# Kernel optimization log

Hardware: AMD Instinct MI355X
Metric: run time of the kernel (lower is better)

The kernel has to match this reference:

```python
import jax, jax.numpy as jnp
import numpy as np

B, D, K, H, E, Z = 64, 25000, 16, 128, 256, 32


def setup_inputs() -> dict:
    key = jax.random.key(0)
    ks = jax.random.split(key, 10)
    s = 0.02
    return {
        "x": jax.random.normal(ks[0], (B, D), jnp.float32),
        "mask": jax.random.randint(ks[1], (B, D), 0, 2, jnp.int32),
        "feat_emb": jax.random.normal(ks[2], (D, K), jnp.float32),          # feature_embedding [D,K]
        "feat_bias": jnp.zeros((D, 1), jnp.float32),                        # feature_bias [D,1]
        "W1": jax.random.normal(ks[3], (1 + K + 1, H), jnp.float32) * s,    # h_layer linear 1 (in,out)
        "b1": jnp.zeros((H,), jnp.float32),
        "W2": jax.random.normal(ks[4], (H, K), jnp.float32) * s,            # h_layer linear 2
        "b2": jnp.zeros((K,), jnp.float32),
        "We1": jax.random.normal(ks[5], (K, E), jnp.float32) * s,           # encoder_mlp linear 1
        "be1": jnp.zeros((E,), jnp.float32),
        "We2": jax.random.normal(ks[6], (E, 2 * Z), jnp.float32) * s,       # encoder_mlp linear 2
        "be2": jnp.zeros((2 * Z,), jnp.float32),
    }


def reference(x, mask, feat_emb, feat_bias, W1, b1, W2, b2, We1, be1, We2, be2):
    b, d = x.shape
    k = feat_emb.shape[1]
    # Build per-(sample, feature) input rows: [x_bd, F_d(K), bias_d] -> [B, D, 1+K+1]
    h_in = jnp.concatenate(
        [
            x[:, :, None],
            jnp.broadcast_to(feat_emb[None, :, :], (b, d, k)),
            jnp.broadcast_to(feat_bias[None, :, :], (b, d, 1)),
        ],
        axis=-1,
    )
    # Shared small MLP (h_layer), dropout is identity at rate 0.0
    h = jax.nn.relu(h_in @ W1 + b1)          # [B, D, H]
    h = jax.nn.relu(h @ W2 + b2)             # [B, D, K]
    # Masked sum pooling over features
    c = jnp.sum(h * mask.astype(h.dtype)[:, :, None], axis=1)  # [B, K]
    # encoder_mlp
    enc = jax.nn.relu(c @ We1 + be1) @ We2 + be2                # [B, 2Z]
    mu, logvar = jnp.split(enc, 2, axis=-1)
    return mu, logvar
```

## Files before the change

### kernel.cpp

```cpp
#include <hip/hip_runtime.h>
#include <hip/hip_bf16.h>

#define B 64
#define D 25000
#define K 16
#define H 128
#define E 256
#define Z 32
#define DTILE 10
#define NBLK (D / DTILE)
#define NREP 8
#define NTILE ((D + 63) / 64)

#define REP_BYTES (NREP * B * K * 4)
#define HI_OFF    REP_BYTES
#define W1F_OFF   (HI_OFF + H * K * 2)
#define XT_OFF    (W1F_OFF + 8 * 64 * 8 * 2)
#define MT_OFF    (XT_OFF + D * B * 2)

typedef __attribute__((ext_vector_type(8))) _Float16 half8;
typedef __attribute__((ext_vector_type(4))) _Float16 hv4;
typedef __attribute__((ext_vector_type(2))) _Float16 hv2;
typedef __attribute__((ext_vector_type(4))) float f32x4;

__global__ __launch_bounds__(256) void prep_kernel(
    const float* __restrict__ x, const int* __restrict__ mask,
    const float* __restrict__ W1, const float* __restrict__ b1,
    const float* __restrict__ W2, float* __restrict__ rep,
    _Float16* __restrict__ hiW2, _Float16* __restrict__ w1f,
    _Float16* __restrict__ xTh, _Float16* __restrict__ mTh)
{
    const int t = threadIdx.x;
    const int bid = blockIdx.x;
    if (bid < NREP) {
        for (int i = t; i < B * K; i += 256) rep[bid * B * K + i] = 0.f;
    } else if (bid == NREP) {
        for (int i = t; i < H * K; i += 256) {
            int j = i & 7, n = (i >> 3) & 15, g = (i >> 7) & 3, s = i >> 9;
            int k = s * 32 + g * 8 + j;
            hiW2[i] = (_Float16)W2[k * K + n];
        }
    } else if (bid == NREP + 1) {
        for (int i = t; i < 8 * 64 * 8; i += 256) {
            int j = i & 7, lane = (i >> 3) & 63, c = i >> 9;
            int g = lane >> 4, n = lane & 15;
            int k = g * 8 + j, h = c * 16 + n;
            float v;
            if (k < 16)       v = W1[(1 + k) * H + h];
            else if (k == 16) v = W1[17 * H + h];
            else if (k == 17) v = b1[h];
            else              v = 0.f;
            w1f[i] = (_Float16)v;
        }
    } else {
        __shared__ float tx[64 * 65];
        __shared__ float tm[64 * 65];
        const int dt0 = (bid - NREP - 2) * 64;
        const int dn  = min(64, D - dt0);
        for (int i = t; i < 64 * 64; i += 256) {
            int bb = i >> 6, dd = i & 63;
            if (dd < dn) {
                tx[dd * 65 + bb] = x[(size_t)bb * D + dt0 + dd];
                tm[dd * 65 + bb] = (float)mask[(size_t)bb * D + dt0 + dd];
            }
        }
        __syncthreads();
        for (int i = t; i < dn * 64; i += 256) {
            int dd = i >> 6, bb = i & 63;
            xTh[(size_t)(dt0 + dd) * 64 + bb] = (_Float16)tx[dd * 65 + bb];
            mTh[(size_t)(dt0 + dd) * 64 + bb] = (_Float16)tm[dd * 65 + bb];
        }
    }
}

__global__ __launch_bounds__(256) void partial_main_kernel(
    const float* __restrict__ feat_emb, const float* __restrict__ feat_bias,
    const float* __restrict__ W1, const float* __restrict__ b2,
    const _Float16* __restrict__ hiW2, const _Float16* __restrict__ w1f,
    const _Float16* __restrict__ xTh, const _Float16* __restrict__ mTh,
    float* __restrict__ rep)
{
    __shared__ __align__(16) _Float16 sGh[DTILE * H];
    __shared__ __align__(16) _Float16 sXh[DTILE * B];
    __shared__ __align__(16) _Float16 sMh[DTILE * B];

    const int t    = threadIdx.x;
    const int d0   = blockIdx.x * DTILE;
    const int lane = t & 63;
    const int wv   = t >> 6;
    const int g    = lane >> 4;
    const int n    = lane & 15;

    {
        const unsigned* xs = (const unsigned*)(xTh + (size_t)d0 * B);
        const unsigned* ms = (const unsigned*)(mTh + (size_t)d0 * B);
        unsigned* xd = (unsigned*)sXh;
        unsigned* md = (unsigned*)sMh;
        for (int i = t; i < DTILE * B / 2; i += 256) { xd[i] = xs[i]; md[i] = ms[i]; }
    }

    {
        const int m  = n;
        const int dA = min(d0 + m, D - 1);
        union AF { half8 v; _Float16 e[8]; } af;
        if (g < 2) {
            const float4* fe = (const float4*)&feat_emb[(size_t)dA * K + g * 8];
            float4 u0 = fe[0], u1 = fe[1];
            af.e[0] = (_Float16)u0.x; af.e[1] = (_Float16)u0.y;
            af.e[2] = (_Float16)u0.z; af.e[3] = (_Float16)u0.w;
            af.e[4] = (_Float16)u1.x; af.e[5] = (_Float16)u1.y;
            af.e[6] = (_Float16)u1.z; af.e[7] = (_Float16)u1.w;
        } else if (g == 2) {
            af.e[0] = (_Float16)feat_bias[dA];
            af.e[1] = (_Float16)1.f;
            #pragma unroll
            for (int j = 2; j < 8; ++j) af.e[j] = (_Float16)0.f;
        } else {
            #pragma unroll
            for (int j = 0; j < 8; ++j) af.e[j] = (_Float16)0.f;
        }
        #pragma unroll
        for (int cc = 0; cc < 2; ++cc) {
            const int c = wv * 2 + cc;
            half8 bf = *(const half8*)(w1f + (((c << 6) + lane) << 3));
            f32x4 C = {0.f, 0.f, 0.f, 0.f};
            C = __builtin_amdgcn_mfma_f32_16x16x32_f16(af.v, bf, C, 0, 0, 0);
            #pragma unroll
            for (int r = 0; r < 4; ++r) {
                const int m2 = g * 4 + r;
                if (m2 < DTILE) sGh[m2 * H + c * 16 + n] = (_Float16)C[r];
            }
        }
    }

    half8 Bf[4];
    #pragma unroll
    for (int s = 0; s < 4; ++s)
        Bf[s] = *(const half8*)(hiW2 + (((s * 4 + g) * 16 + n) << 3));
    hv2 w0h[4][4];
    #pragma unroll
    for (int s = 0; s < 4; ++s) {
        const float4* wp = (const float4*)&W1[s * 32 + g * 8];
        float4 a0 = wp[0], a1 = wp[1];
        w0h[s][0] = (hv2){(_Float16)a0.x, (_Float16)a0.y};
        w0h[s][1] = (hv2){(_Float16)a0.z, (_Float16)a0.w};
        w0h[s][2] = (hv2){(_Float16)a1.x, (_Float16)a1.y};
        w0h[s][3] = (hv2){(_Float16)a1.z, (_Float16)a1.w};
    }
    const float b2n = b2[n];
    const hv2 zeroh = {(_Float16)0.f, (_Float16)0.f};
    __syncthreads();

    const int sample = wv * 16 + n;
    hv2 xh[DTILE / 2];
    #pragma unroll
    for (int i = 0; i < DTILE / 2; ++i)
        xh[i] = (hv2){sXh[(2 * i) * B + sample], sXh[(2 * i + 1) * B + sample]};

    f32x4 cacc = {0.f, 0.f, 0.f, 0.f};
    const int moff = wv * 16 + g * 4;
    const _Float16* gb0 = sGh + g * 8;

    #pragma unroll
    for (int i = 0; i < DTILE / 2; ++i) {
        const int dd0 = 2 * i, dd1 = 2 * i + 1;
        const hv2 xa = {xh[i].x, xh[i].x};
        const hv2 xb = {xh[i].y, xh[i].y};
        f32x4 c1a = {b2n, b2n, b2n, b2n};
        f32x4 c1b = {b2n, b2n, b2n, b2n};
        #pragma unroll
        for (int s = 0; s < 4; ++s) {
            union GA { half8 v; hv2 p[4]; };
            GA ga, gb, A0, A1;
            ga.v = *(const half8*)(gb0 + dd0 * H + s * 32);
            gb.v = *(const half8*)(gb0 + dd1 * H + s * 32);
            #pragma unroll
            for (int p = 0; p < 4; ++p) {
                hv2 h0 = __builtin_elementwise_fma(xa, w0h[s][p], ga.p[p]);
                hv2 h1 = __builtin_elementwise_fma(xb, w0h[s][p], gb.p[p]);
                A0.p[p] = __builtin_elementwise_max(h0, zeroh);
                A1.p[p] = __builtin_elementwise_max(h1, zeroh);
            }
            c1a = __builtin_amdgcn_mfma_f32_16x16x32_f16(A0.v, Bf[s], c1a, 0, 0, 0);
            c1b = __builtin_amdgcn_mfma_f32_16x16x32_f16(A1.v, Bf[s], c1b, 0, 0, 0);
        }
        hv4 m0 = *(const hv4*)&sMh[dd0 * B + moff];
        hv4 m1 = *(const hv4*)&sMh[dd1 * B + moff];
        cacc[0] = fmaf((float)m0.x, fmaxf(c1a[0], 0.f), fmaf((float)m1.x, fmaxf(c1b[0], 0.f), cacc[0]));
        cacc[1] = fmaf((float)m0.y, fmaxf(c1a[1], 0.f), fmaf((float)m1.y, fmaxf(c1b[1], 0.f), cacc[1]));
        cacc[2] = fmaf((float)m0.z, fmaxf(c1a[2], 0.f), fmaf((float)m1.z, fmaxf(c1b[2], 0.f), cacc[2]));
        cacc[3] = fmaf((float)m0.w, fmaxf(c1a[3], 0.f), fmaf((float)m1.w, fmaxf(c1b[3], 0.f), cacc[3]));
    }

    float* crep = rep + (size_t)(blockIdx.x & (NREP - 1)) * (B * K);
    #pragma unroll
    for (int r = 0; r < 4; ++r)
        atomicAdd(&crep[(moff + r) * K + n], cacc[r]);
}

__global__ __launch_bounds__(256) void partial_enc_kernel(
    const float* __restrict__ rep, const float* __restrict__ We1,
    const float* __restrict__ be1, const float* __restrict__ We2,
    const float* __restrict__ be2, float* __restrict__ out)
{
    const int b = blockIdx.x;
    const int t = threadIdx.x;
    __shared__ float sc[K];
    __shared__ float st1[E];
    __shared__ float red[256];

    {
        const int k = t & 15, grp = t >> 4;
        red[t] = (grp < NREP) ? rep[grp * (B * K) + b * K + k] : 0.f;
    }
    __syncthreads();
    if (t < K) {
        float s2 = 0.f;
        #pragma unroll
        for (int q = 0; q < 16; ++q) s2 += red[q * 16 + t];
        sc[t] = s2;
    }
    __syncthreads();

    {
        float acc = be1[t];
        #pragma unroll
        for (int k = 0; k < K; ++k)
            acc = fmaf(sc[k], We1[k * E + t], acc);
        st1[t] = fmaxf(acc, 0.f);
    }
    __syncthreads();

    const int j = t & 63, seg = t >> 6;
    float acc = 0.f;
    #pragma unroll 4
    for (int e = seg * 64; e < seg * 64 + 64; ++e)
        acc = fmaf(st1[e], We2[e * 64 + j], acc);
    red[t] = acc;
    __syncthreads();

    if (t < 64) {
        float v = red[j] + red[64 + j] + red[128 + j] + red[192 + j] + be2[j];
        if (j < Z) out[b * Z + j] = v;
        else       out[B * Z + b * Z + (j - Z)] = v;
    }
}

extern "C" void kernel_launch(void* const* d_in, const int* in_sizes, int n_in,
                              void* d_out, int out_size, void* d_ws, size_t ws_size,
                              hipStream_t stream) {
    const float* x         = (const float*)d_in[0];
    const int*   mask      = (const int*)  d_in[1];
    const float* feat_emb  = (const float*)d_in[2];
    const float* feat_bias = (const float*)d_in[3];
    const float* W1        = (const float*)d_in[4];
    const float* b1        = (const float*)d_in[5];
    const float* W2        = (const float*)d_in[6];
    const float* b2        = (const float*)d_in[7];
    const float* We1       = (const float*)d_in[8];
    const float* be1       = (const float*)d_in[9];
    const float* We2       = (const float*)d_in[10];
    const float* be2       = (const float*)d_in[11];

    float*     rep  = (float*)d_ws;
    _Float16*  hiW2 = (_Float16*)((char*)d_ws + HI_OFF);
    _Float16*  w1f  = (_Float16*)((char*)d_ws + W1F_OFF);
    _Float16*  xTh  = (_Float16*)((char*)d_ws + XT_OFF);
    _Float16*  mTh  = (_Float16*)((char*)d_ws + MT_OFF);

    prep_kernel<<<NREP + 2 + NTILE, 256, 0, stream>>>(
        x, mask, W1, b1, W2, rep, hiW2, w1f, xTh, mTh);
    partial_main_kernel<<<NBLK, 256, 0, stream>>>(
        feat_emb, feat_bias, W1, b2, hiW2, w1f, xTh, mTh, rep);
    partial_enc_kernel<<<B, 256, 0, stream>>>(
        rep, We1, be1, We2, be2, (float*)d_out);
}
```

Measured before the change: 112.9 us.

## Fuse transpose prep into main kernel with double-buffered 16-feature tiles

Removes the separate prep kernel that transposed x/mask to fp16 workspace and pre-swizzled the weights. Each block now loads x and mask directly with vectorized global reads, builds the weight fragments in registers, and processes two 16-feature tiles with double-buffered shared memory so the next tile is staged while the current one is computed. The rep buffer is zeroed with hipMemsetAsync instead. This cuts a full write-and-read pass over the transposed inputs and one launch, but adds per-block weight setup and strided global reads of x/mask.

```diff
diff --git a/kernel.cpp b/kernel.cpp
--- a/kernel.cpp
+++ b/kernel.cpp
@@ -1,5 +1,4 @@
 #include <hip/hip_runtime.h>
-#include <hip/hip_bf16.h>
 
 #define B 64
 #define D 25000
@@ -7,102 +6,109 @@
 #define H 128
 #define E 256
 #define Z 32
-#define DTILE 10
-#define NBLK (D / DTILE)
+#define DTILE 16
+#define NT_TILES 1563
+#define TILES_PER_BLK 2
+#define NPB 782
 #define NREP 8
-#define NTILE ((D + 63) / 64)
+#define XSTR 68
 
 #define REP_BYTES (NREP * B * K * 4)
-#define HI_OFF    REP_BYTES
-#define W1F_OFF   (HI_OFF + H * K * 2)
-#define XT_OFF    (W1F_OFF + 8 * 64 * 8 * 2)
-#define MT_OFF    (XT_OFF + D * B * 2)
 
 typedef __attribute__((ext_vector_type(8))) _Float16 half8;
 typedef __attribute__((ext_vector_type(4))) _Float16 hv4;
 typedef __attribute__((ext_vector_type(2))) _Float16 hv2;
 typedef __attribute__((ext_vector_type(4))) float f32x4;
 
-__global__ __launch_bounds__(256) void prep_kernel(
+__global__ __launch_bounds__(256) void main_kernel(
     const float* __restrict__ x, const int* __restrict__ mask,
+    const float* __restrict__ feat_emb, const float* __restrict__ feat_bias,
     const float* __restrict__ W1, const float* __restrict__ b1,
-    const float* __restrict__ W2, float* __restrict__ rep,
-    _Float16* __restrict__ hiW2, _Float16* __restrict__ w1f,
-    _Float16* __restrict__ xTh, _Float16* __restrict__ mTh)
+    const float* __restrict__ W2, const float* __restrict__ b2,
+    float* __restrict__ rep)
 {
-    const int t = threadIdx.x;
-    const int bid = blockIdx.x;
-    if (bid < NREP) {
-        for (int i = t; i < B * K; i += 256) rep[bid * B * K + i] = 0.f;
-    } else if (bid == NREP) {
-        for (int i = t; i < H * K; i += 256) {
-            int j = i & 7, n = (i >> 3) & 15, g = (i >> 7) & 3, s = i >> 9;
-            int k = s * 32 + g * 8 + j;
-            hiW2[i] = (_Float16)W2[k * K + n];
-        }
-    } else if (bid == NREP + 1) {
-        for (int i = t; i < 8 * 64 * 8; i += 256) {
-            int j = i & 7, lane = (i >> 3) & 63, c = i >> 9;
-            int g = lane >> 4, n = lane & 15;
-            int k = g * 8 + j, h = c * 16 + n;
+    __shared__ __align__(16) _Float16 sGh[2][DTILE * H];
+    __shared__ __align__(16) _Float16 sXh[2][DTILE * XSTR];
+    __shared__ __align__(16) _Float16 sMh[2][DTILE * XSTR];
+
+    const int t    = threadIdx.x;
+    const int lane = t & 63;
+    const int wv   = t >> 6;
+    const int g    = lane >> 4;
+    const int n    = lane & 15;
+
+    half8 Bf[4];
+    #pragma unroll
+    for (int s = 0; s < 4; ++s) {
+        union { half8 v; _Float16 e[8]; } u;
+        #pragma unroll
+        for (int j = 0; j < 8; ++j)
+            u.e[j] = (_Float16)W2[(s * 32 + g * 8 + j) * K + n];
+        Bf[s] = u.v;
+    }
+    hv2 w0h[4][4];
+    #pragma unroll
+    for (int s = 0; s < 4; ++s) {
+        const float4* wp = (const float4*)&W1[s * 32 + g * 8];
+        float4 a0 = wp[0], a1 = wp[1];
+        w0h[s][0] = (hv2){(_Float16)a0.x, (_Float16)a0.y};
+        w0h[s][1] = (hv2){(_Float16)a0.z, (_Float16)a0.w};
+        w0h[s][2] = (hv2){(_Float16)a1.x, (_Float16)a1.y};
+        w0h[s][3] = (hv2){(_Float16)a1.z, (_Float16)a1.w};
+    }
+    half8 bfG[2];
+    #pragma unroll
+    for (int cc = 0; cc < 2; ++cc) {
+        const int h = (wv * 2 + cc) * 16 + n;
+        union { half8 v; _Float16 e[8]; } u;
+        #pragma unroll
+        for (int j = 0; j < 8; ++j) {
+            const int k = g * 8 + j;
             float v;
             if (k < 16)       v = W1[(1 + k) * H + h];
             else if (k == 16) v = W1[17 * H + h];
             else if (k == 17) v = b1[h];
             else              v = 0.f;
-            w1f[i] = (_Float16)v;
-        }
-    } else {
-        __shared__ float tx[64 * 65];
-        __shared__ float tm[64 * 65];
-        const int dt0 = (bid - NREP - 2) * 64;
-        const int dn  = min(64, D - dt0);
-        for (int i = t; i < 64 * 64; i += 256) {
-            int bb = i >> 6, dd = i & 63;
-            if (dd < dn) {
-                tx[dd * 65 + bb] = x[(size_t)bb * D + dt0 + dd];
-                tm[dd * 65 + bb] = (float)mask[(size_t)bb * D + dt0 + dd];
+            u.e[j] = (_Float16)v;
+        }
+        bfG[cc] = u.v;
+    }
+    const float b2n = b2[n];
+    const hv2 zeroh = {(_Float16)0.f, (_Float16)0.f};
+    const int moff = wv * 16 + g * 4;
+    const int sample = wv * 16 + n;
+
+    const int t0 = blockIdx.x * TILES_PER_BLK;
+    const int t1 = min(t0 + TILES_PER_BLK, NT_TILES);
+
+    auto STAGE = [&](int buf, int tile) {
+        const int bb = t >> 2;
+        const int dd = (t & 3) * 4;
+        const int dg = tile * DTILE + dd;
+        float xv[4], mv[4];
+        if (dg + 4 <= D) {
+            float4 xx = *(const float4*)&x[(size_t)bb * D + dg];
+            int4   mm = *(const int4*)&mask[(size_t)bb * D + dg];
+            xv[0] = xx.x; xv[1] = xx.y; xv[2] = xx.z; xv[3] = xx.w;
+            mv[0] = (float)mm.x; mv[1] = (float)mm.y; mv[2] = (float)mm.z; mv[3] = (float)mm.w;
+        } else {
+            #pragma unroll
+            for (int i = 0; i < 4; ++i) {
+                const int dgi = dg + i;
+                xv[i] = (dgi < D) ? x[(size_t)bb * D + dgi] : 0.f;
+                mv[i] = (dgi < D) ? (float)mask[(size_t)bb * D + dgi] : 0.f;
             }
         }
-        __syncthreads();
-        for (int i = t; i < dn * 64; i += 256) {
-            int dd = i >> 6, bb = i & 63;
-            xTh[(size_t)(dt0 + dd) * 64 + bb] = (_Float16)tx[dd * 65 + bb];
-            mTh[(size_t)(dt0 + dd) * 64 + bb] = (_Float16)tm[dd * 65 + bb];
-        }
-    }
-}
-
-__global__ __launch_bounds__(256) void partial_main_kernel(
-    const float* __restrict__ feat_emb, const float* __restrict__ feat_bias,
-    const float* __restrict__ W1, const float* __restrict__ b2,
-    const _Float16* __restrict__ hiW2, const _Float16* __restrict__ w1f,
-    const _Float16* __restrict__ xTh, const _Float16* __restrict__ mTh,
-    float* __restrict__ rep)
-{
-    __shared__ __align__(16) _Float16 sGh[DTILE * H];
-    __shared__ __align__(16) _Float16 sXh[DTILE * B];
-    __shared__ __align__(16) _Float16 sMh[DTILE * B];
-
-    const int t    = threadIdx.x;
-    const int d0   = blockIdx.x * DTILE;
-    const int lane = t & 63;
-    const int wv   = t >> 6;
-    const int g    = lane >> 4;
-    const int n    = lane & 15;
-
-    {
-        const unsigned* xs = (const unsigned*)(xTh + (size_t)d0 * B);
-        const unsigned* ms = (const unsigned*)(mTh + (size_t)d0 * B);
-        unsigned* xd = (unsigned*)sXh;
-        unsigned* md = (unsigned*)sMh;
-        for (int i = t; i < DTILE * B / 2; i += 256) { xd[i] = xs[i]; md[i] = ms[i]; }
-    }
-
-    {
-        const int m  = n;
-        const int dA = min(d0 + m, D - 1);
-        union AF { half8 v; _Float16 e[8]; } af;
+        #pragma unroll
+        for (int i = 0; i < 4; ++i) {
+            sXh[buf][(dd + i) * XSTR + bb] = (_Float16)xv[i];
+            sMh[buf][(dd + i) * XSTR + bb] = (_Float16)mv[i];
+        }
+    };
+
+    auto GCOMP = [&](int buf, int tile) {
+        const int dA = min(tile * DTILE + n, D - 1);
+        union { half8 v; _Float16 e[8]; } af;
         if (g < 2) {
             const float4* fe = (const float4*)&feat_emb[(size_t)dA * K + g * 8];
             float4 u0 = fe[0], u1 = fe[1];
@@ -121,75 +127,63 @@
         }
         #pragma unroll
         for (int cc = 0; cc < 2; ++cc) {
-            const int c = wv * 2 + cc;
-            half8 bf = *(const half8*)(w1f + (((c << 6) + lane) << 3));
             f32x4 C = {0.f, 0.f, 0.f, 0.f};
-            C = __builtin_amdgcn_mfma_f32_16x16x32_f16(af.v, bf, C, 0, 0, 0);
-            #pragma unroll
-            for (int r = 0; r < 4; ++r) {
-                const int m2 = g * 4 + r;
-                if (m2 < DTILE) sGh[m2 * H + c * 16 + n] = (_Float16)C[r];
+            C = __builtin_amdgcn_mfma_f32_16x16x32_f16(af.v, bfG[cc], C, 0, 0, 0);
+            #pragma unroll
+            for (int r = 0; r < 4; ++r)
+                sGh[buf][(g * 4 + r) * H + (wv * 2 + cc) * 16 + n] = (_Float16)C[r];
+        }
+    };
+
+    f32x4 cacc = {0.f, 0.f, 0.f, 0.f};
+
+    STAGE(0, t0);
+    GCOMP(0, t0);
+    __syncthreads();
+
+    int cur = 0;
+    for (int tt = t0; tt < t1; ++tt) {
+        if (tt + 1 < t1) { STAGE(cur ^ 1, tt + 1); GCOMP(cur ^ 1, tt + 1); }
+
+        hv2 xh[DTILE / 2];
+        #pragma unroll
+        for (int i = 0; i < DTILE / 2; ++i)
+            xh[i] = (hv2){sXh[cur][(2 * i) * XSTR + sample],
+                          sXh[cur][(2 * i + 1) * XSTR + sample]};
+        const _Float16* gb0 = sGh[cur] + g * 8;
+
+        #pragma unroll
+        for (int i = 0; i < DTILE / 2; ++i) {
+            const int dd0 = 2 * i, dd1 = 2 * i + 1;
+            const hv2 xa = {xh[i].x, xh[i].x};
+            const hv2 xb = {xh[i].y, xh[i].y};
+            f32x4 c1a = {b2n, b2n, b2n, b2n};
+            f32x4 c1b = {b2n, b2n, b2n, b2n};
+            #pragma unroll
+            for (int s = 0; s < 4; ++s) {
+                union GA { half8 v; hv2 p[4]; };
+                GA ga, gb, A0, A1;
+                ga.v = *(const half8*)(gb0 + dd0 * H + s * 32);
+                gb.v = *(const half8*)(gb0 + dd1 * H + s * 32);
+                #pragma unroll
+                for (int p = 0; p < 4; ++p) {
+                    hv2 h0 = __builtin_elementwise_fma(xa, w0h[s][p], ga.p[p]);
+                    hv2 h1 = __builtin_elementwise_fma(xb, w0h[s][p], gb.p[p]);
+                    A0.p[p] = __builtin_elementwise_max(h0, zeroh);
+                    A1.p[p] = __builtin_elementwise_max(h1, zeroh);
+                }
+                c1a = __builtin_amdgcn_mfma_f32_16x16x32_f16(A0.v, Bf[s], c1a, 0, 0, 0);
+                c1b = __builtin_amdgcn_mfma_f32_16x16x32_f16(A1.v, Bf[s], c1b, 0, 0, 0);
             }
-        }
-    }
-
-    half8 Bf[4];
-    #pragma unroll
-    for (int s = 0; s < 4; ++s)
-        Bf[s] = *(const half8*)(hiW2 + (((s * 4 + g) * 16 + n) << 3));
-    hv2 w0h[4][4];
-    #pragma unroll
-    for (int s = 0; s < 4; ++s) {
-        const float4* wp = (const float4*)&W1[s * 32 + g * 8];
-        float4 a0 = wp[0], a1 = wp[1];
-        w0h[s][0] = (hv2){(_Float16)a0.x, (_Float16)a0.y};
-        w0h[s][1] = (hv2){(_Float16)a0.z, (_Float16)a0.w};
-        w0h[s][2] = (hv2){(_Float16)a1.x, (_Float16)a1.y};
-        w0h[s][3] = (hv2){(_Float16)a1.z, (_Float16)a1.w};
-    }
-    const float b2n = b2[n];
-    const hv2 zeroh = {(_Float16)0.f, (_Float16)0.f};
-    __syncthreads();
-
-    const int sample = wv * 16 + n;
-    hv2 xh[DTILE / 2];
-    #pragma unroll
-    for (int i = 0; i < DTILE / 2; ++i)
-        xh[i] = (hv2){sXh[(2 * i) * B + sample], sXh[(2 * i + 1) * B + sample]};
-
-    f32x4 cacc = {0.f, 0.f, 0.f, 0.f};
-    const int moff = wv * 16 + g * 4;
-    const _Float16* gb0 = sGh + g * 8;
-
-    #pragma unroll
-    for (int i = 0; i < DTILE / 2; ++i) {
-        const int dd0 = 2 * i, dd1 = 2 * i + 1;
-        const hv2 xa = {xh[i].x, xh[i].x};
-        const hv2 xb = {xh[i].y, xh[i].y};
-        f32x4 c1a = {b2n, b2n, b2n, b2n};
-        f32x4 c1b = {b2n, b2n, b2n, b2n};
-        #pragma unroll
-        for (int s = 0; s < 4; ++s) {
-            union GA { half8 v; hv2 p[4]; };
-            GA ga, gb, A0, A1;
-            ga.v = *(const half8*)(gb0 + dd0 * H + s * 32);
-            gb.v = *(const half8*)(gb0 + dd1 * H + s * 32);
-            #pragma unroll
-            for (int p = 0; p < 4; ++p) {
-                hv2 h0 = __builtin_elementwise_fma(xa, w0h[s][p], ga.p[p]);
-                hv2 h1 = __builtin_elementwise_fma(xb, w0h[s][p], gb.p[p]);
-                A0.p[p] = __builtin_elementwise_max(h0, zeroh);
-                A1.p[p] = __builtin_elementwise_max(h1, zeroh);
-            }
-            c1a = __builtin_amdgcn_mfma_f32_16x16x32_f16(A0.v, Bf[s], c1a, 0, 0, 0);
-            c1b = __builtin_amdgcn_mfma_f32_16x16x32_f16(A1.v, Bf[s], c1b, 0, 0, 0);
-        }
-        hv4 m0 = *(const hv4*)&sMh[dd0 * B + moff];
-        hv4 m1 = *(const hv4*)&sMh[dd1 * B + moff];
-        cacc[0] = fmaf((float)m0.x, fmaxf(c1a[0], 0.f), fmaf((float)m1.x, fmaxf(c1b[0], 0.f), cacc[0]));
-        cacc[1] = fmaf((float)m0.y, fmaxf(c1a[1], 0.f), fmaf((float)m1.y, fmaxf(c1b[1], 0.f), cacc[1]));
-        cacc[2] = fmaf((float)m0.z, fmaxf(c1a[2], 0.f), fmaf((float)m1.z, fmaxf(c1b[2], 0.f), cacc[2]));
-        cacc[3] = fmaf((float)m0.w, fmaxf(c1a[3], 0.f), fmaf((float)m1.w, fmaxf(c1b[3], 0.f), cacc[3]));
+            hv4 m0 = *(const hv4*)&sMh[cur][dd0 * XSTR + moff];
+            hv4 m1 = *(const hv4*)&sMh[cur][dd1 * XSTR + moff];
+            cacc[0] = fmaf((float)m0.x, fmaxf(c1a[0], 0.f), fmaf((float)m1.x, fmaxf(c1b[0], 0.f), cacc[0]));
+            cacc[1] = fmaf((float)m0.y, fmaxf(c1a[1], 0.f), fmaf((float)m1.y, fmaxf(c1b[1], 0.f), cacc[1]));
+            cacc[2] = fmaf((float)m0.z, fmaxf(c1a[2], 0.f), fmaf((float)m1.z, fmaxf(c1b[2], 0.f), cacc[2]));
+            cacc[3] = fmaf((float)m0.w, fmaxf(c1a[3], 0.f), fmaf((float)m1.w, fmaxf(c1b[3], 0.f), cacc[3]));
+        }
+        __syncthreads();
+        cur ^= 1;
     }
 
     float* crep = rep + (size_t)(blockIdx.x & (NREP - 1)) * (B * K);
@@ -262,16 +256,11 @@
     const float* We2       = (const float*)d_in[10];
     const float* be2       = (const float*)d_in[11];
 
-    float*     rep  = (float*)d_ws;
-    _Float16*  hiW2 = (_Float16*)((char*)d_ws + HI_OFF);
-    _Float16*  w1f  = (_Float16*)((char*)d_ws + W1F_OFF);
-    _Float16*  xTh  = (_Float16*)((char*)d_ws + XT_OFF);
-    _Float16*  mTh  = (_Float16*)((char*)d_ws + MT_OFF);
-
-    prep_kernel<<<NREP + 2 + NTILE, 256, 0, stream>>>(
-        x, mask, W1, b1, W2, rep, hiW2, w1f, xTh, mTh);
-    partial_main_kernel<<<NBLK, 256, 0, stream>>>(
-        feat_emb, feat_bias, W1, b2, hiW2, w1f, xTh, mTh, rep);
+    float* rep = (float*)d_ws;
+
+    hipMemsetAsync(rep, 0, REP_BYTES, stream);
+    main_kernel<<<NPB, 256, 0, stream>>>(
+        x, mask, feat_emb, feat_bias, W1, b1, W2, b2, rep);
     partial_enc_kernel<<<B, 256, 0, stream>>>(
         rep, We1, be1, We2, be2, (float*)d_out);
 }
```

After: 115.6 us. 1.02x slower.
